# Kernel optimization log

Hardware: AMD Instinct MI355X
Metric: run time of the kernel (lower is better)

Reference implementation:

```python
import math
import jax, jax.numpy as jnp
import numpy as np

N_EMBD = 1024
N_HEAD = 16
HEAD_DIM = N_EMBD // N_HEAD


def setup_inputs() -> dict:
    key = jax.random.key(0)
    k1, k2, k3, k4, k5 = jax.random.split(key, 5)
    B, T, C = 1, 4096, N_EMBD
    s = 1.0 / math.sqrt(C)
    return {
        "x": jax.random.normal(k1, (B, T, C), dtype=jnp.float32),
        "w_qkv": jax.random.normal(k2, (C, 3 * C), dtype=jnp.float32) * s,
        "b_qkv": jnp.zeros((3 * C,), dtype=jnp.float32),
        "w_proj": jax.random.normal(k3, (C, C), dtype=jnp.float32) * s,
        "b_proj": jnp.zeros((C,), dtype=jnp.float32),
    }


def reference(x, w_qkv, b_qkv, w_proj, b_proj):
    B, T, C = x.shape
    qkv = x @ w_qkv + b_qkv                       # [B,T,3C]
    q, k, v = jnp.split(qkv, 3, axis=-1)
    # [B,T,C] -> [B,H,T,D]
    def heads(t):
        return t.reshape(B, T, N_HEAD, HEAD_DIM).transpose(0, 2, 1, 3)
    q, k, v = heads(q), heads(k), heads(v)
    scale = 1.0 / math.sqrt(HEAD_DIM)
    attn = jnp.einsum("bhqd,bhkd->bhqk", q, k) * scale
    causal = jnp.tril(jnp.ones((T, T), dtype=bool))
    attn = jnp.where(causal, attn, -jnp.inf)
    attn = jax.nn.softmax(attn, axis=-1)
    out = jnp.einsum("bhqk,bhkd->bhqd", attn, v)   # [B,H,T,D]
    out = out.transpose(0, 2, 1, 3).reshape(B, T, C)
    return out @ w_proj + b_proj
```

## Files before the change

kernel.cpp:

```cpp
#include <hip/hip_runtime.h>
#include <hip/hip_bf16.h>

#define TT 4096
#define CC 1024
#define NHEAD 16
#define DH 64
#define N3C 3072

typedef __attribute__((ext_vector_type(8))) short short8;
typedef __attribute__((ext_vector_type(4))) float floatx4;
typedef __attribute__((ext_vector_type(4))) unsigned int uint4v;

#define QSCALE 0.18033688011112042f

__device__ __forceinline__ short f2bf(float f) {
    union { __hip_bfloat16 h; short s; } u;
    u.h = __float2bfloat16(f);
    return u.s;
}

__device__ __forceinline__ void gload_lds16(const void* g, void* l) {
    __builtin_amdgcn_global_load_lds(
        (const __attribute__((address_space(1))) unsigned int*)(unsigned long long)g,
        (__attribute__((address_space(3))) unsigned int*)(unsigned int)(unsigned long long)l,
        16, 0, 0);
}

__device__ __forceinline__ unsigned pk_trunc(float lo, float hi) {
    return __builtin_amdgcn_perm(__float_as_uint(hi), __float_as_uint(lo), 0x07060302u);
}

__device__ __forceinline__ unsigned pk_rne(float lo, float hi) {
    unsigned a = (unsigned short)f2bf(lo);
    unsigned b = (unsigned short)f2bf(hi);
    return a | (b << 16);
}

__device__ __forceinline__ void tr_body(const float* __restrict__ in, short* __restrict__ out,
                                        int K, int N, int bx, int by, int tid, float (*tile)[33]) {
    int nt = bx * 32, kt = by * 32;
    int tx = tid & 31, ty = tid >> 5;
#pragma unroll
    for (int i = 0; i < 32; i += 8)
        tile[ty + i][tx] = in[(size_t)(kt + ty + i) * N + nt + tx];
    __syncthreads();
#pragma unroll
    for (int i = 0; i < 32; i += 8)
        out[(size_t)(nt + ty + i) * K + kt + tx] = f2bf(tile[tx][ty + i]);
}

__global__ void k_prep(const float* __restrict__ x, short* __restrict__ xb,
                       const float* __restrict__ w_qkv, short* __restrict__ wqkvT,
                       const float* __restrict__ w_proj, short* __restrict__ wprojT) {
    __shared__ float tile[32][33];
    int id = blockIdx.x;
    int tid = threadIdx.x;
    if (id < 4096) {
        int i = (id * 256 + tid) * 4;
        float4 v = *(const float4*)&x[i];
        short4 r;
        r.x = f2bf(v.x); r.y = f2bf(v.y); r.z = f2bf(v.z); r.w = f2bf(v.w);
        *(short4*)&xb[i] = r;
    } else if (id < 4096 + 3072) {
        int r = id - 4096;
        tr_body(w_qkv, wqkvT, CC, N3C, r % 96, r / 96, tid, tile);
    } else {
        int r = id - 7168;
        tr_body(w_proj, wprojT, CC, CC, r & 31, r >> 5, tid, tile);
    }
}

__global__ __launch_bounds__(256) void k_gemm_qkv(const short* __restrict__ A,
                                                  const short* __restrict__ Bt,
                                                  const float* __restrict__ bias,
                                                  short* __restrict__ Q,
                                                  short* __restrict__ Kb,
                                                  short* __restrict__ Vtg) {
    const int m0 = blockIdx.y * 128;
    const int n0 = blockIdx.x * 128;
    __shared__ __attribute__((aligned(16))) short Sbuf[4][128 * 32];
    const int tid = threadIdx.x;
    const int lane = tid & 63;
    const int w = tid >> 6;
    const int wm = w >> 1, wn = w & 1;
    const int quad = lane >> 4;
    const int l16 = lane & 15;

    const int r0 = tid >> 2, c0 = (tid & 3) * 8;
    const short* pA[2][2]; const short* pB[2][2];
    short* lA[2][2]; short* lB[2][2];
#pragma unroll
    for (int it = 0; it < 2; ++it)
#pragma unroll
        for (int hh = 0; hh < 2; ++hh) {
            pA[it][hh] = A + (size_t)(m0 + it * 64 + r0) * CC + hh * 32 + c0;
            pB[it][hh] = Bt + (size_t)(n0 + it * 64 + r0) * CC + hh * 32 + c0;
            lA[it][hh] = &Sbuf[hh][(it * 256 + w * 64) * 8];
            lB[it][hh] = &Sbuf[2 + hh][(it * 256 + w * 64) * 8];
        }

    floatx4 acc[4][4] = {};
    for (int kb = 0; kb < CC; kb += 64) {
        __syncthreads();
#pragma unroll
        for (int it = 0; it < 2; ++it)
#pragma unroll
            for (int hh = 0; hh < 2; ++hh) {
                gload_lds16(pA[it][hh] + kb, lA[it][hh]);
                gload_lds16(pB[it][hh] + kb, lB[it][hh]);
            }
        __syncthreads();
#pragma unroll
        for (int kk = 0; kk < 2; ++kk) {
            short8 af[4], bf[4];
#pragma unroll
            for (int mi = 0; mi < 4; ++mi)
                af[mi] = *(const short8*)&Sbuf[kk][(wm * 64 + mi * 16 + l16) * 32 + quad * 8];
#pragma unroll
            for (int ni = 0; ni < 4; ++ni)
                bf[ni] = *(const short8*)&Sbuf[2 + kk][(wn * 64 + ni * 16 + l16) * 32 + quad * 8];
#pragma unroll
            for (int mi = 0; mi < 4; ++mi)
#pragma unroll
                for (int ni = 0; ni < 4; ++ni)
                    acc[mi][ni] = __builtin_amdgcn_mfma_f32_16x16x32_bf16(af[mi], bf[ni], acc[mi][ni], 0, 0, 0);
        }
    }

    __syncthreads();
    char* T = (char*)&Sbuf[0][0];
    const int which = n0 >> 10;

    if (which < 2) {
        const float sc = (which == 0) ? QSCALE : 1.0f;
#pragma unroll
        for (int mi = 0; mi < 4; ++mi)
#pragma unroll
            for (int ni = 0; ni < 4; ++ni) {
                int nl = wn * 64 + ni * 16 + l16;
                float bv = bias[n0 + nl];
#pragma unroll
                for (int r = 0; r < 4; ++r) {
                    int ml = wm * 64 + mi * 16 + quad * 4 + r;
                    *(short*)(T + ml * 256 + ((nl * 2) ^ ((ml & 7) << 4))) =
                        f2bf((acc[mi][ni][r] + bv) * sc);
                }
            }
        __syncthreads();
        short* base = (which == 0) ? Q : Kb;
        const int row = tid >> 4, seg = tid & 15;
#pragma unroll
        for (int p = 0; p < 8; ++p) {
            int m = p * 16 + row;
            uint4v v = *(uint4v*)(T + m * 256 + ((seg * 16) ^ ((m & 7) << 4)));
            int gn = n0 + seg * 8 - which * 1024;
            int hh2 = gn >> 6, d = gn & 63;
            *(uint4v*)&base[((size_t)hh2 * TT + (m0 + m)) * DH + d] = v;
        }
    } else {
#pragma unroll
        for (int mi = 0; mi < 4; ++mi)
#pragma unroll
            for (int ni = 0; ni < 4; ++ni) {
                int nl = wn * 64 + ni * 16 + l16;
                float bv = bias[n0 + nl];
                int ml0 = wm * 64 + mi * 16 + quad * 4;
                uint2 pk;
                pk.x = pk_rne(acc[mi][ni][0] + bv, acc[mi][ni][1] + bv);
                pk.y = pk_rne(acc[mi][ni][2] + bv, acc[mi][ni][3] + bv);
                *(uint2*)(T + nl * 256 + ((ml0 * 2) ^ ((nl & 7) << 4))) = pk;
            }
        __syncthreads();
        const int row = tid >> 4, seg = tid & 15;
#pragma unroll
        for (int p = 0; p < 8; ++p) {
            int n = p * 16 + row;
            uint4v v = *(uint4v*)(T + n * 256 + ((seg * 16) ^ ((n & 7) << 4)));
            int gn = n0 + n - 2048;
            int hh2 = gn >> 6, d = gn & 63;
            *(uint4v*)&Vtg[((size_t)hh2 * DH + d) * TT + m0 + seg * 8] = v;
        }
    }
}

__device__ __forceinline__ void attn_tile(const short* __restrict__ Qp,
                                          const short* __restrict__ Kp,
                                          const short* __restrict__ Vp,
                                          short* __restrict__ Ob,
                                          int h, int qi,
                                          int tid, int lane, int w, int quad, int l16,
                                          short* __restrict__ Ps0,
                                          float (*wl)[64], float* lsum) {
    const int q0 = qi * 64;
    const int nk = (qi >> 1) + 1;

    short8 aq[4][2];
#pragma unroll
    for (int qg = 0; qg < 4; ++qg)
#pragma unroll
        for (int ss = 0; ss < 2; ++ss)
            aq[qg][ss] = *(const short8*)&Qp[(size_t)(q0 + qg * 16 + l16) * DH + ss * 32 + quad * 8];

    floatx4 accO[4] = {};
    float l_part[4] = {0.f, 0.f, 0.f, 0.f};
    int buf = 0;

    short8 kf[2][2];
#pragma unroll
    for (int mi = 0; mi < 2; ++mi)
#pragma unroll
        for (int ss = 0; ss < 2; ++ss)
            kf[mi][ss] = *(const short8*)&Kp[(size_t)(w * 32 + mi * 16 + l16) * DH + ss * 32 + quad * 8];

    for (int ki = 0; ki < nk; ++ki) {
        const int k0 = ki * 128;
        const bool masked = (ki == nk - 1);

        floatx4 accS[2][4] = {};
        __builtin_amdgcn_s_setprio(1);
#pragma unroll
        for (int mi = 0; mi < 2; ++mi)
#pragma unroll
            for (int ss = 0; ss < 2; ++ss)
#pragma unroll
                for (int qg = 0; qg < 4; ++qg)
                    accS[mi][qg] = __builtin_amdgcn_mfma_f32_16x16x32_bf16(kf[mi][ss], aq[qg][ss], accS[mi][qg], 0, 0, 0);
        __builtin_amdgcn_s_setprio(0);

        short* Pb = Ps0 + buf * (64 * 136);
#pragma unroll
        for (int mi = 0; mi < 2; ++mi) {
            const int kbase = k0 + w * 32 + mi * 16 + quad * 4;
#pragma unroll
            for (int qg = 0; qg < 4; ++qg) {
                float pv[4];
#pragma unroll
                for (int r = 0; r < 4; ++r) {
                    float e = __builtin_amdgcn_exp2f(accS[mi][qg][r]);
                    if (masked)
                        e = (kbase + r <= q0 + qg * 16 + l16) ? e : 0.f;
                    pv[r] = e;
                    l_part[qg] += e;
                }
                uint2 pk;
                pk.x = pk_trunc(pv[0], pv[1]);
                pk.y = pk_trunc(pv[2], pv[3]);
                *(uint2*)&Pb[(qg * 16 + l16) * 136 + w * 32 + mi * 16 + quad * 4] = pk;
            }
        }

        short8 vf[4];
#pragma unroll
        for (int ks = 0; ks < 4; ++ks)
            vf[ks] = *(const short8*)&Vp[(size_t)(w * 16 + l16) * TT + k0 + ks * 32 + quad * 8];

        short8 kfn[2][2];
        if (ki + 1 < nk) {
            const int kn0 = k0 + 128;
#pragma unroll
            for (int mi = 0; mi < 2; ++mi)
#pragma unroll
                for (int ss = 0; ss < 2; ++ss)
                    kfn[mi][ss] = *(const short8*)&Kp[(size_t)(kn0 + w * 32 + mi * 16 + l16) * DH + ss * 32 + quad * 8];
        }

        asm volatile("s_waitcnt lgkmcnt(0)" ::: "memory");
        __builtin_amdgcn_s_barrier();
        asm volatile("" ::: "memory");

        __builtin_amdgcn_s_setprio(1);
#pragma unroll
        for (int qg = 0; qg < 4; ++qg)
#pragma unroll
            for (int ks = 0; ks < 4; ++ks) {
                short8 ap = *(const short8*)&Pb[(qg * 16 + l16) * 136 + ks * 32 + quad * 8];
                accO[qg] = __builtin_amdgcn_mfma_f32_16x16x32_bf16(ap, vf[ks], accO[qg], 0, 0, 0);
            }
        __builtin_amdgcn_s_setprio(0);

#pragma unroll
        for (int mi = 0; mi < 2; ++mi)
#pragma unroll
            for (int ss = 0; ss < 2; ++ss)
                kf[mi][ss] = kfn[mi][ss];
        buf ^= 1;
    }

#pragma unroll
    for (int qg = 0; qg < 4; ++qg) {
        float lr = l_part[qg];
        lr += __shfl_xor(lr, 16, 64);
        lr += __shfl_xor(lr, 32, 64);
        if (lane < 16) wl[w][qg * 16 + lane] = lr;
    }
    __syncthreads();
    if (tid < 64) lsum[tid] = wl[0][tid] + wl[1][tid] + wl[2][tid] + wl[3][tid];
    __syncthreads();

#pragma unroll
    for (int qg = 0; qg < 4; ++qg) {
#pragma unroll
        for (int r = 0; r < 4; ++r) {
            int q = qg * 16 + quad * 4 + r;
            float o = accO[qg][r] / lsum[q];
            Ob[(size_t)(q0 + q) * CC + h * DH + w * 16 + l16] = f2bf(o);
        }
    }
}

__global__ __launch_bounds__(256) void k_attn(const short* __restrict__ Qh,
                                              const short* __restrict__ Kh,
                                              const short* __restrict__ VhT,
                                              short* __restrict__ Ob) {
    const int h = blockIdx.x;
    const int y = blockIdx.y;
    const int tid = threadIdx.x, lane = tid & 63, w = tid >> 6;
    const int quad = lane >> 4, l16 = lane & 15;

    __shared__ __attribute__((aligned(16))) short Ps[2][64 * 136];
    __shared__ float wl[4][64];
    __shared__ float lsum[64];

    const short* Qp = Qh + (size_t)h * TT * DH;
    const short* Kp = Kh + (size_t)h * TT * DH;
    const short* Vp = VhT + (size_t)h * DH * TT;

    attn_tile(Qp, Kp, Vp, Ob, h, 63 - y, tid, lane, w, quad, l16, &Ps[0][0], wl, lsum);
    attn_tile(Qp, Kp, Vp, Ob, h, y,      tid, lane, w, quad, l16, &Ps[0][0], wl, lsum);
}

__global__ __launch_bounds__(256) void k_gemm_proj(const short* __restrict__ A,
                                                   const short* __restrict__ Bt,
                                                   const float* __restrict__ bias,
                                                   float* __restrict__ out) {
    const int m0 = blockIdx.y * 64;
    const int n0 = blockIdx.x * 128;
    __shared__ __attribute__((aligned(16))) short As[2][64 * 32];
    __shared__ __attribute__((aligned(16))) short Bs[2][128 * 32];
    const int tid = threadIdx.x;
    const int lane = tid & 63;
    const int w = tid >> 6;
    const int quad = lane >> 4;
    const int l16 = lane & 15;

    const int r0 = tid >> 2, c0 = (tid & 3) * 8;
    const short* pA[2]; const short* pB[2][2];
    short* lA[2]; short* lB[2][2];
#pragma unroll
    for (int hh = 0; hh < 2; ++hh) {
        pA[hh] = A + (size_t)(m0 + r0) * CC + hh * 32 + c0;
        lA[hh] = &As[hh][w * 512];
#pragma unroll
        for (int it = 0; it < 2; ++it) {
            pB[it][hh] = Bt + (size_t)(n0 + it * 64 + r0) * CC + hh * 32 + c0;
            lB[it][hh] = &Bs[hh][(it * 256 + w * 64) * 8];
        }
    }

    floatx4 acc[4][2] = {};
    for (int kb = 0; kb < CC; kb += 64) {
        __syncthreads();
#pragma unroll
        for (int hh = 0; hh < 2; ++hh) {
            gload_lds16(pA[hh] + kb, lA[hh]);
#pragma unroll
            for (int it = 0; it < 2; ++it)
                gload_lds16(pB[it][hh] + kb, lB[it][hh]);
        }
        __syncthreads();
#pragma unroll
        for (int kk = 0; kk < 2; ++kk) {
            short8 af[4], bf[2];
#pragma unroll
            for (int mi = 0; mi < 4; ++mi)
                af[mi] = *(const short8*)&As[kk][(mi * 16 + l16) * 32 + quad * 8];
#pragma unroll
            for (int ni = 0; ni < 2; ++ni)
                bf[ni] = *(const short8*)&Bs[kk][(w * 32 + ni * 16 + l16) * 32 + quad * 8];
#pragma unroll
            for (int mi = 0; mi < 4; ++mi)
#pragma unroll
                for (int ni = 0; ni < 2; ++ni)
                    acc[mi][ni] = __builtin_amdgcn_mfma_f32_16x16x32_bf16(af[mi], bf[ni], acc[mi][ni], 0, 0, 0);
        }
    }
#pragma unroll
    for (int mi = 0; mi < 4; ++mi) {
#pragma unroll
        for (int ni = 0; ni < 2; ++ni) {
            int gm = m0 + mi * 16 + quad * 4;
            int gn = n0 + w * 32 + ni * 16 + l16;
            float bv = bias[gn];
#pragma unroll
            for (int r = 0; r < 4; ++r)
                out[(size_t)(gm + r) * CC + gn] = acc[mi][ni][r] + bv;
        }
    }
}

extern "C" void kernel_launch(void* const* d_in, const int* in_sizes, int n_in,
                              void* d_out, int out_size, void* d_ws, size_t ws_size,
                              hipStream_t stream) {
    const float* x      = (const float*)d_in[0];
    const float* w_qkv  = (const float*)d_in[1];
    const float* b_qkv  = (const float*)d_in[2];
    const float* w_proj = (const float*)d_in[3];
    const float* b_proj = (const float*)d_in[4];
    float* out = (float*)d_out;
    char* ws = (char*)d_ws;

    short* xb     = (short*)(ws);
    short* wqkvT  = (short*)(ws + 8388608);
    short* wprojT = (short*)(ws + 14680064);
    short* Qh     = (short*)(ws + 16777216);
    short* Kh     = (short*)(ws + 25165824);
    short* VhT    = (short*)(ws + 33554432);
    short* Ob     = (short*)(ws + 41943040);

    k_prep<<<8192, 256, 0, stream>>>(x, xb, w_qkv, wqkvT, w_proj, wprojT);
    k_gemm_qkv<<<dim3(N3C / 128, TT / 128), 256, 0, stream>>>(xb, wqkvT, b_qkv, Qh, Kh, VhT);
    k_attn<<<dim3(NHEAD, 32), 256, 0, stream>>>(Qh, Kh, VhT, Ob);
    k_gemm_proj<<<dim3(CC / 128, TT / 64), 256, 0, stream>>>(Ob, wprojT, b_proj, out);
}
```

Measured before the change: 208.8 us.

## Restructure attention to 32x32 MFMA with LDS-staged K/V and register-resident P

Rewrites the attention kernel so each wave owns 32 query rows and iterates over 64-key tiles. K and V tiles are staged into double-buffered, XOR-swizzled LDS via direct global-to-LDS loads, and 32x32x16 MFMAs are used. The P matrix stays in registers, rearranged with permlane32 swaps instead of a round trip through LDS, and the cross-wave row-sum reduction is dropped. The grid is halved to 16x16 blocks of 128-query tiles, which gives fewer blocks and per-wave causal skip logic, with possible occupancy and load-balance changes.

```diff
diff --git a/kernel.cpp b/kernel.cpp
--- a/kernel.cpp
+++ b/kernel.cpp
@@ -9,6 +9,7 @@
 
 typedef __attribute__((ext_vector_type(8))) short short8;
 typedef __attribute__((ext_vector_type(4))) float floatx4;
+typedef __attribute__((ext_vector_type(16))) float floatx16;
 typedef __attribute__((ext_vector_type(4))) unsigned int uint4v;
 
 #define QSCALE 0.18033688011112042f
@@ -183,128 +184,139 @@
     }
 }
 
-__device__ __forceinline__ void attn_tile(const short* __restrict__ Qp,
-                                          const short* __restrict__ Kp,
-                                          const short* __restrict__ Vp,
-                                          short* __restrict__ Ob,
-                                          int h, int qi,
-                                          int tid, int lane, int w, int quad, int l16,
-                                          short* __restrict__ Ps0,
-                                          float (*wl)[64], float* lsum) {
-    const int q0 = qi * 64;
-    const int nk = (qi >> 1) + 1;
-
-    short8 aq[4][2];
-#pragma unroll
-    for (int qg = 0; qg < 4; ++qg)
-#pragma unroll
-        for (int ss = 0; ss < 2; ++ss)
-            aq[qg][ss] = *(const short8*)&Qp[(size_t)(q0 + qg * 16 + l16) * DH + ss * 32 + quad * 8];
-
-    floatx4 accO[4] = {};
-    float l_part[4] = {0.f, 0.f, 0.f, 0.f};
+__device__ __forceinline__ void stage_kv(const short* __restrict__ Kp,
+                                         const short* __restrict__ Vp,
+                                         short* lk, short* lv,
+                                         int k0, int w, int lane) {
+    const int p = lane & 7;
+    const int rl = lane >> 3;
+#pragma unroll
+    for (int i = 0; i < 2; ++i) {
+        const int R = w * 16 + i * 8 + rl;
+        const int u = p ^ (R & 7);
+        gload_lds16(Kp + (size_t)(k0 + R) * DH + u * 8, lk + (w * 16 + i * 8) * 64);
+        gload_lds16(Vp + (size_t)R * TT + k0 + u * 8,   lv + (w * 16 + i * 8) * 64);
+    }
+}
+
+__device__ __forceinline__ void attn_qtile(const short* __restrict__ Qp,
+                                           const short* __restrict__ Kp,
+                                           const short* __restrict__ Vp,
+                                           short* __restrict__ Ob,
+                                           int h, int qi,
+                                           int w, int lane, int l31, int hi,
+                                           short* ldsK, short* ldsV) {
+    const int qs = qi * 128 + w * 32;
+    const int nk = 2 * qi + 2;
+
+    short8 bq[4];
+#pragma unroll
+    for (int st = 0; st < 4; ++st)
+        bq[st] = *(const short8*)&Qp[(size_t)(qs + l31) * DH + st * 16 + hi * 8];
+
+    floatx16 accO0 = {}, accO1 = {};
+    float l_acc = 0.f;
+
+    stage_kv(Kp, Vp, ldsK, ldsV, 0, w, lane);
+    asm volatile("s_waitcnt vmcnt(0)" ::: "memory");
+    __builtin_amdgcn_s_barrier();
+    asm volatile("" ::: "memory");
+
     int buf = 0;
-
-    short8 kf[2][2];
-#pragma unroll
-    for (int mi = 0; mi < 2; ++mi)
-#pragma unroll
-        for (int ss = 0; ss < 2; ++ss)
-            kf[mi][ss] = *(const short8*)&Kp[(size_t)(w * 32 + mi * 16 + l16) * DH + ss * 32 + quad * 8];
-
-    for (int ki = 0; ki < nk; ++ki) {
-        const int k0 = ki * 128;
-        const bool masked = (ki == nk - 1);
-
-        floatx4 accS[2][4] = {};
-        __builtin_amdgcn_s_setprio(1);
-#pragma unroll
-        for (int mi = 0; mi < 2; ++mi)
-#pragma unroll
-            for (int ss = 0; ss < 2; ++ss)
-#pragma unroll
-                for (int qg = 0; qg < 4; ++qg)
-                    accS[mi][qg] = __builtin_amdgcn_mfma_f32_16x16x32_bf16(kf[mi][ss], aq[qg][ss], accS[mi][qg], 0, 0, 0);
-        __builtin_amdgcn_s_setprio(0);
-
-        short* Pb = Ps0 + buf * (64 * 136);
-#pragma unroll
-        for (int mi = 0; mi < 2; ++mi) {
-            const int kbase = k0 + w * 32 + mi * 16 + quad * 4;
-#pragma unroll
-            for (int qg = 0; qg < 4; ++qg) {
-                float pv[4];
-#pragma unroll
-                for (int r = 0; r < 4; ++r) {
-                    float e = __builtin_amdgcn_exp2f(accS[mi][qg][r]);
-                    if (masked)
-                        e = (kbase + r <= q0 + qg * 16 + l16) ? e : 0.f;
-                    pv[r] = e;
-                    l_part[qg] += e;
+    for (int t = 0; t < nk; ++t) {
+        const int k0 = t * 64;
+        if (t + 1 < nk)
+            stage_kv(Kp, Vp, ldsK + (buf ^ 1) * 4096, ldsV + (buf ^ 1) * 4096,
+                     k0 + 64, w, lane);
+
+        const bool skip = (k0 > qs + 31);
+        if (!skip) {
+            const short* lk = ldsK + buf * 4096;
+            const short* lv = ldsV + buf * 4096;
+            const bool masked = (k0 + 63 > qs);
+            const int qg = qs + l31;
+
+            short8 ak[2][4];
+#pragma unroll
+            for (int sub = 0; sub < 2; ++sub)
+#pragma unroll
+                for (int st = 0; st < 4; ++st)
+                    ak[sub][st] = *(const short8*)&lk[(sub * 32 + l31) * 64 +
+                                                     (((st * 2 + hi) ^ (l31 & 7)) * 8)];
+
+            floatx16 s0 = {}, s1 = {};
+#pragma unroll
+            for (int st = 0; st < 4; ++st) {
+                s0 = __builtin_amdgcn_mfma_f32_32x32x16_bf16(ak[0][st], bq[st], s0, 0, 0, 0);
+                s1 = __builtin_amdgcn_mfma_f32_32x32x16_bf16(ak[1][st], bq[st], s1, 0, 0, 0);
+            }
+
+#pragma unroll
+            for (int sub = 0; sub < 2; ++sub) {
+                float p[16];
+#pragma unroll
+                for (int r = 0; r < 16; ++r)
+                    p[r] = __builtin_amdgcn_exp2f(sub == 0 ? s0[r] : s1[r]);
+                if (masked) {
+#pragma unroll
+                    for (int r = 0; r < 16; ++r) {
+                        int kg = k0 + sub * 32 + (r & 3) + 8 * (r >> 2) + 4 * hi;
+                        p[r] = (kg <= qg) ? p[r] : 0.f;
+                    }
                 }
-                uint2 pk;
-                pk.x = pk_trunc(pv[0], pv[1]);
-                pk.y = pk_trunc(pv[2], pv[3]);
-                *(uint2*)&Pb[(qg * 16 + l16) * 136 + w * 32 + mi * 16 + quad * 4] = pk;
+                {
+                    float t0 = (p[0] + p[1]) + (p[2] + p[3]);
+                    float t1 = (p[4] + p[5]) + (p[6] + p[7]);
+                    float t2 = (p[8] + p[9]) + (p[10] + p[11]);
+                    float t3 = (p[12] + p[13]) + (p[14] + p[15]);
+                    l_acc += (t0 + t1) + (t2 + t3);
+                }
+                unsigned pa[8];
+                pa[0] = pk_trunc(p[0], p[1]);   pa[1] = pk_trunc(p[2], p[3]);
+                pa[2] = pk_trunc(p[4], p[5]);   pa[3] = pk_trunc(p[6], p[7]);
+                pa[4] = pk_trunc(p[8], p[9]);   pa[5] = pk_trunc(p[10], p[11]);
+                pa[6] = pk_trunc(p[12], p[13]); pa[7] = pk_trunc(p[14], p[15]);
+                asm("v_permlane32_swap_b32 %0, %1" : "+v"(pa[0]), "+v"(pa[2]));
+                asm("v_permlane32_swap_b32 %0, %1" : "+v"(pa[1]), "+v"(pa[3]));
+                asm("v_permlane32_swap_b32 %0, %1" : "+v"(pa[4]), "+v"(pa[6]));
+                asm("v_permlane32_swap_b32 %0, %1" : "+v"(pa[5]), "+v"(pa[7]));
+                uint4v a0v = {pa[0], pa[1], pa[2], pa[3]};
+                uint4v a1v = {pa[4], pa[5], pa[6], pa[7]};
+                short8 A0 = __builtin_bit_cast(short8, a0v);
+                short8 A1 = __builtin_bit_cast(short8, a1v);
+
+                short8 vf00 = *(const short8*)&lv[(l31) * 64 +
+                                                  (((sub * 4 + hi) ^ (l31 & 7)) * 8)];
+                short8 vf01 = *(const short8*)&lv[(l31) * 64 +
+                                                  (((sub * 4 + 2 + hi) ^ (l31 & 7)) * 8)];
+                short8 vf10 = *(const short8*)&lv[(32 + l31) * 64 +
+                                                  (((sub * 4 + hi) ^ (l31 & 7)) * 8)];
+                short8 vf11 = *(const short8*)&lv[(32 + l31) * 64 +
+                                                  (((sub * 4 + 2 + hi) ^ (l31 & 7)) * 8)];
+
+                accO0 = __builtin_amdgcn_mfma_f32_32x32x16_bf16(A0, vf00, accO0, 0, 0, 0);
+                accO0 = __builtin_amdgcn_mfma_f32_32x32x16_bf16(A1, vf01, accO0, 0, 0, 0);
+                accO1 = __builtin_amdgcn_mfma_f32_32x32x16_bf16(A0, vf10, accO1, 0, 0, 0);
+                accO1 = __builtin_amdgcn_mfma_f32_32x32x16_bf16(A1, vf11, accO1, 0, 0, 0);
             }
         }
 
-        short8 vf[4];
-#pragma unroll
-        for (int ks = 0; ks < 4; ++ks)
-            vf[ks] = *(const short8*)&Vp[(size_t)(w * 16 + l16) * TT + k0 + ks * 32 + quad * 8];
-
-        short8 kfn[2][2];
-        if (ki + 1 < nk) {
-            const int kn0 = k0 + 128;
-#pragma unroll
-            for (int mi = 0; mi < 2; ++mi)
-#pragma unroll
-                for (int ss = 0; ss < 2; ++ss)
-                    kfn[mi][ss] = *(const short8*)&Kp[(size_t)(kn0 + w * 32 + mi * 16 + l16) * DH + ss * 32 + quad * 8];
-        }
-
-        asm volatile("s_waitcnt lgkmcnt(0)" ::: "memory");
+        asm volatile("s_waitcnt vmcnt(0)" ::: "memory");
         __builtin_amdgcn_s_barrier();
         asm volatile("" ::: "memory");
-
-        __builtin_amdgcn_s_setprio(1);
-#pragma unroll
-        for (int qg = 0; qg < 4; ++qg)
-#pragma unroll
-            for (int ks = 0; ks < 4; ++ks) {
-                short8 ap = *(const short8*)&Pb[(qg * 16 + l16) * 136 + ks * 32 + quad * 8];
-                accO[qg] = __builtin_amdgcn_mfma_f32_16x16x32_bf16(ap, vf[ks], accO[qg], 0, 0, 0);
-            }
-        __builtin_amdgcn_s_setprio(0);
-
-#pragma unroll
-        for (int mi = 0; mi < 2; ++mi)
-#pragma unroll
-            for (int ss = 0; ss < 2; ++ss)
-                kf[mi][ss] = kfn[mi][ss];
         buf ^= 1;
     }
 
-#pragma unroll
-    for (int qg = 0; qg < 4; ++qg) {
-        float lr = l_part[qg];
-        lr += __shfl_xor(lr, 16, 64);
-        lr += __shfl_xor(lr, 32, 64);
-        if (lane < 16) wl[w][qg * 16 + lane] = lr;
-    }
-    __syncthreads();
-    if (tid < 64) lsum[tid] = wl[0][tid] + wl[1][tid] + wl[2][tid] + wl[3][tid];
-    __syncthreads();
-
-#pragma unroll
-    for (int qg = 0; qg < 4; ++qg) {
-#pragma unroll
-        for (int r = 0; r < 4; ++r) {
-            int q = qg * 16 + quad * 4 + r;
-            float o = accO[qg][r] / lsum[q];
-            Ob[(size_t)(q0 + q) * CC + h * DH + w * 16 + l16] = f2bf(o);
-        }
+    l_acc += __shfl_xor(l_acc, 32, 64);
+    float inv = __builtin_amdgcn_rcpf(l_acc);
+
+#pragma unroll
+    for (int r = 0; r < 16; ++r) {
+        int qr = (r & 3) + 8 * (r >> 2) + 4 * hi;
+        float iv = __shfl(inv, qr, 64);
+        int qg = qs + qr;
+        Ob[(size_t)qg * CC + h * DH + l31]      = f2bf(accO0[r] * iv);
+        Ob[(size_t)qg * CC + h * DH + 32 + l31] = f2bf(accO1[r] * iv);
     }
 }
 
@@ -314,19 +326,21 @@
                                               short* __restrict__ Ob) {
     const int h = blockIdx.x;
     const int y = blockIdx.y;
-    const int tid = threadIdx.x, lane = tid & 63, w = tid >> 6;
-    const int quad = lane >> 4, l16 = lane & 15;
-
-    __shared__ __attribute__((aligned(16))) short Ps[2][64 * 136];
-    __shared__ float wl[4][64];
-    __shared__ float lsum[64];
+    const int tid = threadIdx.x;
+    const int w = tid >> 6;
+    const int lane = tid & 63;
+    const int l31 = lane & 31;
+    const int hi = lane >> 5;
+
+    __shared__ __attribute__((aligned(16))) short ldsK[2][4096];
+    __shared__ __attribute__((aligned(16))) short ldsV[2][4096];
 
     const short* Qp = Qh + (size_t)h * TT * DH;
     const short* Kp = Kh + (size_t)h * TT * DH;
     const short* Vp = VhT + (size_t)h * DH * TT;
 
-    attn_tile(Qp, Kp, Vp, Ob, h, 63 - y, tid, lane, w, quad, l16, &Ps[0][0], wl, lsum);
-    attn_tile(Qp, Kp, Vp, Ob, h, y,      tid, lane, w, quad, l16, &Ps[0][0], wl, lsum);
+    attn_qtile(Qp, Kp, Vp, Ob, h, 31 - y, w, lane, l31, hi, &ldsK[0][0], &ldsV[0][0]);
+    attn_qtile(Qp, Kp, Vp, Ob, h, y,      w, lane, l31, hi, &ldsK[0][0], &ldsV[0][0]);
 }
 
 __global__ __launch_bounds__(256) void k_gemm_proj(const short* __restrict__ A,
@@ -419,6 +433,6 @@
 
     k_prep<<<8192, 256, 0, stream>>>(x, xb, w_qkv, wqkvT, w_proj, wprojT);
     k_gemm_qkv<<<dim3(N3C / 128, TT / 128), 256, 0, stream>>>(xb, wqkvT, b_qkv, Qh, Kh, VhT);
-    k_attn<<<dim3(NHEAD, 32), 256, 0, stream>>>(Qh, Kh, VhT, Ob);
+    k_attn<<<dim3(NHEAD, 16), 256, 0, stream>>>(Qh, Kh, VhT, Ob);
     k_gemm_proj<<<dim3(CC / 128, TT / 64), 256, 0, stream>>>(Ob, wprojT, b_proj, out);
 }
```

Measured after the change: 206.6 us. No clear change (-1.1%).
